# Kernel tuning notes

Hardware: AMD Instinct MI355X
Metric: run time of the kernel (lower is better)

The kernel has to match this reference:

```python
import jax, jax.numpy as jnp
import numpy as np

DIM = 64
SQRT_DIM = float(np.sqrt(DIM))


def setup_inputs() -> dict:
    rng = jax.random.key(0)
    k1, k2, k3, k4 = jax.random.split(rng, 4)
    B, S, D = 16, 2048, DIM
    query = jax.random.normal(k1, (B, S, D), dtype=jnp.float32)
    key = jax.random.normal(k2, (B, S, D), dtype=jnp.float32)
    value = jax.random.normal(k3, (B, S, D), dtype=jnp.float32)
    mask = jax.random.randint(k4, (B, S), 0, 2) == 1  # True = masked (pad)
    return {"query": query, "key": key, "value": value, "mask": mask}


def reference(query, key, value, mask):
    # score: [B, S, S]
    score = jnp.einsum('bsd,btd->bst', query, key) / SQRT_DIM
    # symmetric mask: position (i, j) masked if token i OR token j is padded
    m = jnp.logical_or(mask[:, :, None], mask[:, None, :])  # [B, S, S]
    score = jnp.where(m, -jnp.inf, score)
    attn = jax.nn.softmax(score, axis=-1)
    attn = jnp.where(m, 0.0, attn)
    context = jnp.einsum('bst,btd->bsd', attn, value)
    return (context, attn)
```

## Files before the change

kernel.cpp:

```cpp
#include <hip/hip_runtime.h>
#include <hip/hip_bf16.h>

#define NBATCH 16
#define SLEN   2048
#define DIM    64
#define TQ     64
#define NTHR   256
#define NW     4
#define PANEL  128
#define NPANEL (SLEN / PANEL)
#define PROWP  136
#define PROWK  72
#define PROWV  136

typedef __attribute__((ext_vector_type(8))) short bf16x8;
typedef __attribute__((ext_vector_type(4))) float f32x4;

__device__ inline short f2bf(float f) {
    union { __hip_bfloat16 h; short s; } u;
    u.h = __float2bfloat16(f);
    return u.s;
}
__device__ inline float bf2f(unsigned short s) {
    union { unsigned u; float f; } x;
    x.u = ((unsigned)s) << 16;
    return x.f;
}
__device__ inline bf16x8 pack8(float4 a, float4 b) {
    bf16x8 r;
    r[0] = f2bf(a.x); r[1] = f2bf(a.y); r[2] = f2bf(a.z); r[3] = f2bf(a.w);
    r[4] = f2bf(b.x); r[5] = f2bf(b.y); r[6] = f2bf(b.z); r[7] = f2bf(b.w);
    return r;
}
__device__ inline bf16x8 pack8s(float4 a, float4 b, float s) {
    bf16x8 r;
    r[0] = f2bf(a.x * s); r[1] = f2bf(a.y * s); r[2] = f2bf(a.z * s); r[3] = f2bf(a.w * s);
    r[4] = f2bf(b.x * s); r[5] = f2bf(b.y * s); r[6] = f2bf(b.z * s); r[7] = f2bf(b.w * s);
    return r;
}

__global__ __launch_bounds__(256) void preconvert_kernel(
    const float* __restrict__ K, const float* __restrict__ V,
    short* __restrict__ Kws, short* __restrict__ Vp)
{
    const int b  = blockIdx.x >> 4;
    const int p  = blockIdx.x & 15;
    const int j0 = p * PANEL;
    const int tid = threadIdx.x;
    const float* Kb = K + ((size_t)b * SLEN + j0) * DIM;
    const float* Vb = V + ((size_t)b * SLEN + j0) * DIM;
    short* Kwb = Kws + ((size_t)b * SLEN + j0) * DIM;
    short* Vpb = Vp  + (size_t)b * SLEN * DIM + (size_t)p * 8192;

    #pragma unroll
    for (int it = 0; it < 8; it++) {
        const int idx = it * 256 + tid;
        const int row = idx >> 4, c4 = idx & 15;
        float4 kv = *(const float4*)(Kb + (size_t)row * DIM + c4 * 4);
        const int blk = (c4 >> 1) ^ (row & 7);
        *(short4*)(Kwb + (size_t)row * DIM + blk * 8 + (c4 & 1) * 4) =
            make_short4(f2bf(kv.x), f2bf(kv.y), f2bf(kv.z), f2bf(kv.w));
    }
    #pragma unroll
    for (int it = 0; it < 2; it++) {
        const int task = it * 256 + tid;
        const int kb = (task >> 4) * 4, d4 = (task & 15) * 4;
        const float* vp = Vb + (size_t)kb * DIM + d4;
        float4 r0 = *(const float4*)(vp);
        float4 r1 = *(const float4*)(vp + DIM);
        float4 r2 = *(const float4*)(vp + 2 * DIM);
        float4 r3 = *(const float4*)(vp + 3 * DIM);
        const int ks = (kb >> 5) & 3, gg = (kb >> 3) & 3, e = kb & 7;
        #define VDST(dd) (Vpb + ((size_t)((ks * 4 + ((d4 + dd) >> 4)) * 64 \
                              + gg * 16 + ((d4 + dd) & 15))) * 8 + e)
        *(short4*)VDST(0) = make_short4(f2bf(r0.x), f2bf(r1.x), f2bf(r2.x), f2bf(r3.x));
        *(short4*)VDST(1) = make_short4(f2bf(r0.y), f2bf(r1.y), f2bf(r2.y), f2bf(r3.y));
        *(short4*)VDST(2) = make_short4(f2bf(r0.z), f2bf(r1.z), f2bf(r2.z), f2bf(r3.z));
        *(short4*)VDST(3) = make_short4(f2bf(r0.w), f2bf(r1.w), f2bf(r2.w), f2bf(r3.w));
        #undef VDST
    }
}

__device__ __forceinline__ void stage_k_panel(const short* __restrict__ Kwb, int j0,
                                              short* sdst, int w, int l) {
    const short* src = Kwb + (size_t)j0 * DIM + w * 512 + l * 8;
    short* dst = sdst + w * 512;
    #pragma unroll
    for (int i = 0; i < 4; i++)
        __builtin_amdgcn_global_load_lds((const unsigned int*)(src + i * 2048),
                                         (unsigned int*)(dst + i * 2048), 16, 0, 0);
}

#define MFMA16(a, bb, cc) __builtin_amdgcn_mfma_f32_16x16x32_bf16((a), (bb), (cc), 0, 0, 0)

__global__ __launch_bounds__(NTHR, 3) void sdpa_kernel(
    const float* __restrict__ Q, const short* __restrict__ Kws,
    const short* __restrict__ Vp, const int* __restrict__ M,
    float* __restrict__ outCtx, float* __restrict__ outAttn)
{
    __shared__ __align__(16) short sK0[PANEL * DIM];
    __shared__ __align__(16) short sK1[PANEL * DIM];
    __shared__ __align__(16) short sP[NW * 16 * PROWP];
    __shared__ short sMaskBf[SLEN];

    const int tid = threadIdx.x;
    const int w = tid >> 6, l = tid & 63, g = l >> 4, c = l & 15;
    const int wg = (blockIdx.x & 7) * (NBATCH * (SLEN / TQ) / 8) + (blockIdx.x >> 3);
    const int b  = wg >> 5;
    const int i0 = (wg & 31) * TQ;
    const int i0w = i0 + w * 16;

    const short* Kwb = Kws + (size_t)b * SLEN * DIM;
    const short* Vwb = Vp  + (size_t)b * SLEN * DIM;
    const int*   Mb  = M + b * SLEN;

    bf16x8 qa0, qa1;
    {
        const float* qp = Q + ((size_t)b * SLEN + i0w + c) * DIM + g * 8;
        qa0 = pack8s(*(const float4*)(qp),      *(const float4*)(qp + 4),  0.125f);
        qa1 = pack8s(*(const float4*)(qp + 32), *(const float4*)(qp + 36), 0.125f);
    }

    stage_k_panel(Kwb, 0, sK0, w, l);
    #pragma unroll
    for (int i = 0; i < 8; i++) {
        const int idx = i * NTHR + tid;
        sMaskBf[idx] = Mb[idx] ? (short)0 : (short)0x3F80;
    }
    __syncthreads();

    float rsum[4] = {0.f, 0.f, 0.f, 0.f};
    for (int p = 0; p < NPANEL; p++) {
        const short* cur = (p & 1) ? sK1 : sK0;
        if (p < NPANEL - 1)
            stage_k_panel(Kwb, (p + 1) * PANEL, (p & 1) ? sK0 : sK1, w, l);
        const int j0 = p * PANEL;
        #pragma unroll
        for (int jt = 0; jt < 8; jt++) {
            const short* kr = cur + (jt * 16 + c) * DIM;
            bf16x8 kb0 = *(const bf16x8*)(kr + ((g ^ (c & 7)) * 8));
            bf16x8 kb1 = *(const bf16x8*)(kr + (((g + 4) ^ (c & 7)) * 8));
            f32x4 acc = {0.f, 0.f, 0.f, 0.f};
            acc = MFMA16(qa0, kb0, acc);
            acc = MFMA16(qa1, kb1, acc);
            const float em = bf2f((unsigned short)sMaskBf[j0 + jt * 16 + c]);
            #pragma unroll
            for (int r = 0; r < 4; r++)
                rsum[r] += __expf(acc[r]) * em;
        }
        __syncthreads();
    }

    stage_k_panel(Kwb, 0, sK0, w, l);

    #pragma unroll
    for (int off = 1; off < 16; off <<= 1) {
        #pragma unroll
        for (int r = 0; r < 4; r++)
            rsum[r] += __shfl_xor(rsum[r], off, 64);
    }
    float scv[4];
    #pragma unroll
    for (int r = 0; r < 4; r++) {
        const bool rm = sMaskBf[i0w + g * 4 + r] == 0;
        scv[r] = (rm || rsum[r] <= 0.f) ? 0.f : 1.f / rsum[r];
    }

    short* sPw = sP + w * 16 * PROWP;
    f32x4 pv[4];
    #pragma unroll
    for (int nt = 0; nt < 4; nt++) pv[nt] = (f32x4){0.f, 0.f, 0.f, 0.f};

    __syncthreads();

    for (int p = 0; p < NPANEL; p++) {
        const int j0 = p * PANEL;
        if (p < NPANEL - 1)
            stage_k_panel(Kwb, j0 + PANEL, (p & 1) ? sK0 : sK1, w, l);
        const short* kbuf = (p & 1) ? sK1 : sK0;

        #pragma unroll
        for (int jt = 0; jt < 8; jt++) {
            const short* kr = kbuf + (jt * 16 + c) * DIM;
            bf16x8 kb0 = *(const bf16x8*)(kr + ((g ^ (c & 7)) * 8));
            bf16x8 kb1 = *(const bf16x8*)(kr + (((g + 4) ^ (c & 7)) * 8));
            f32x4 acc = {0.f, 0.f, 0.f, 0.f};
            acc = MFMA16(qa0, kb0, acc);
            acc = MFMA16(qa1, kb1, acc);
            const float em = bf2f((unsigned short)sMaskBf[j0 + jt * 16 + c]);
            #pragma unroll
            for (int r = 0; r < 4; r++)
                sPw[(g * 4 + r) * PROWP + jt * 16 + c] =
                    f2bf(__expf(acc[r]) * em * scv[r]);
        }
        {
            const short* vb = Vwb + (size_t)p * 8192 + l * 8;
            bf16x8 v0 = *(const bf16x8*)(vb);
            bf16x8 v1 = *(const bf16x8*)(vb + 512);
            bf16x8 af;
            #pragma unroll
            for (int i = 0; i < 16; i++) {
                bf16x8 cur = v0;
                v0 = v1;
                if (i + 2 < 16) v1 = *(const bf16x8*)(vb + (i + 2) * 512);
                if ((i & 3) == 0)
                    af = *(const bf16x8*)(sPw + c * PROWP + (i >> 2) * 32 + g * 8);
                pv[i & 3] = MFMA16(af, cur, pv[i & 3]);
            }
        }
        const size_t rowBase = (size_t)b * SLEN + i0w;
        #pragma unroll
        for (int it = 0; it < 8; it++) {
            const int idx = it * 64 + l;
            const int row = idx >> 5, col4 = idx & 31;
            const unsigned short* pp = (const unsigned short*)sPw + row * PROWP + col4 * 4;
            ushort4 p4 = *(const ushort4*)(pp);
            f32x4 o = {bf2f(p4.x), bf2f(p4.y), bf2f(p4.z), bf2f(p4.w)};
            __builtin_nontemporal_store(o,
                (f32x4*)(outAttn + (rowBase + row) * SLEN + j0 + col4 * 4));
        }
        __syncthreads();
    }

    #pragma unroll
    for (int nt = 0; nt < 4; nt++) {
        #pragma unroll
        for (int r = 0; r < 4; r++)
            __builtin_nontemporal_store(pv[nt][r],
                outCtx + ((size_t)b * SLEN + i0w + g * 4 + r) * DIM + nt * 16 + c);
    }
}

__global__ __launch_bounds__(NTHR, 3) void sdpa_kernel_fb(
    const float* __restrict__ Q, const float* __restrict__ K,
    const float* __restrict__ V, const int* __restrict__ M,
    float* __restrict__ outCtx, float* __restrict__ outAttn)
{
    __shared__ __align__(16) short sK[128 * PROWK];
    __shared__ __align__(16) short sVT[64 * PROWV];
    __shared__ __align__(16) short sP[NW * 16 * PROWP];
    __shared__ float sMask[PANEL];

    const int tid = threadIdx.x;
    const int w = tid >> 6, l = tid & 63, g = l >> 4, c = l & 15;
    const int b  = blockIdx.x >> 5;
    const int i0 = (blockIdx.x & 31) * TQ;
    const int i0w = i0 + w * 16;

    const float* Kb = K + (size_t)b * SLEN * DIM;
    const float* Vb = V + (size_t)b * SLEN * DIM;
    const int*   Mb = M + b * SLEN;

    bf16x8 qa0, qa1;
    {
        const float* qp = Q + ((size_t)b * SLEN + i0w + c) * DIM + g * 8;
        qa0 = pack8(*(const float4*)(qp),      *(const float4*)(qp + 4));
        qa1 = pack8(*(const float4*)(qp + 32), *(const float4*)(qp + 36));
    }

    const float scl = 0.125f;
    float rsum[4] = {0.f, 0.f, 0.f, 0.f};

    for (int p = 0; p < NPANEL; p++) {
        const int j0 = p * PANEL;
        #pragma unroll
        for (int it = 0; it < 8; it++) {
            const int idx = it * NTHR + tid;
            const int row = idx >> 4, c4 = idx & 15;
            float4 kv = *(const float4*)(Kb + (size_t)(j0 + row) * DIM + c4 * 4);
            *(short4*)(sK + row * PROWK + c4 * 4) =
                make_short4(f2bf(kv.x), f2bf(kv.y), f2bf(kv.z), f2bf(kv.w));
        }
        if (tid < PANEL) sMask[tid] = Mb[j0 + tid] ? 0.f : 1.f;
        __syncthreads();
        #pragma unroll
        for (int jt = 0; jt < 8; jt++) {
            const short* kr = sK + (jt * 16 + c) * PROWK + g * 8;
            bf16x8 kb0 = *(const bf16x8*)(kr);
            bf16x8 kb1 = *(const bf16x8*)(kr + 32);
            f32x4 acc = {0.f, 0.f, 0.f, 0.f};
            acc = MFMA16(qa0, kb0, acc);
            acc = MFMA16(qa1, kb1, acc);
            const float em = sMask[jt * 16 + c];
            #pragma unroll
            for (int r = 0; r < 4; r++)
                rsum[r] += __expf(acc[r] * scl) * em;
        }
        __syncthreads();
    }
    #pragma unroll
    for (int off = 1; off < 16; off <<= 1) {
        #pragma unroll
        for (int r = 0; r < 4; r++)
            rsum[r] += __shfl_xor(rsum[r], off, 64);
    }
    float scv[4];
    #pragma unroll
    for (int r = 0; r < 4; r++) {
        const int rm = Mb[i0w + g * 4 + r];
        scv[r] = (rm || rsum[r] <= 0.f) ? 0.f : 1.f / rsum[r];
    }

    short* sPw = sP + w * 16 * PROWP;
    f32x4 pv[4];
    #pragma unroll
    for (int nt = 0; nt < 4; nt++) pv[nt] = (f32x4){0.f, 0.f, 0.f, 0.f};

    for (int p = 0; p < NPANEL; p++) {
        const int j0 = p * PANEL;
        #pragma unroll
        for (int it = 0; it < 8; it++) {
            const int idx = it * NTHR + tid;
            const int row = idx >> 4, c4 = idx & 15;
            float4 kv = *(const float4*)(Kb + (size_t)(j0 + row) * DIM + c4 * 4);
            *(short4*)(sK + row * PROWK + c4 * 4) =
                make_short4(f2bf(kv.x), f2bf(kv.y), f2bf(kv.z), f2bf(kv.w));
        }
        #pragma unroll
        for (int it = 0; it < 2; it++) {
            const int task = it * NTHR + tid;
            const int k4 = task >> 4, d4g = task & 15;
            const int kb = k4 * 4, d4 = d4g * 4;
            const int colb = kb ^ ((d4g & 3) << 3);
            const float* vp = Vb + (size_t)(j0 + kb) * DIM + d4;
            float4 r0 = *(const float4*)(vp);
            float4 r1 = *(const float4*)(vp + DIM);
            float4 r2 = *(const float4*)(vp + 2 * DIM);
            float4 r3 = *(const float4*)(vp + 3 * DIM);
            *(short4*)(sVT + (d4 + 0) * PROWV + colb) =
                make_short4(f2bf(r0.x), f2bf(r1.x), f2bf(r2.x), f2bf(r3.x));
            *(short4*)(sVT + (d4 + 1) * PROWV + colb) =
                make_short4(f2bf(r0.y), f2bf(r1.y), f2bf(r2.y), f2bf(r3.y));
            *(short4*)(sVT + (d4 + 2) * PROWV + colb) =
                make_short4(f2bf(r0.z), f2bf(r1.z), f2bf(r2.z), f2bf(r3.z));
            *(short4*)(sVT + (d4 + 3) * PROWV + colb) =
                make_short4(f2bf(r0.w), f2bf(r1.w), f2bf(r2.w), f2bf(r3.w));
        }
        if (tid < PANEL) sMask[tid] = Mb[j0 + tid] ? 0.f : 1.f;
        __syncthreads();

        #pragma unroll
        for (int jt = 0; jt < 8; jt++) {
            const short* kr = sK + (jt * 16 + c) * PROWK + g * 8;
            bf16x8 kb0 = *(const bf16x8*)(kr);
            bf16x8 kb1 = *(const bf16x8*)(kr + 32);
            f32x4 acc = {0.f, 0.f, 0.f, 0.f};
            acc = MFMA16(qa0, kb0, acc);
            acc = MFMA16(qa1, kb1, acc);
            const float em = sMask[jt * 16 + c];
            #pragma unroll
            for (int r = 0; r < 4; r++)
                sPw[(g * 4 + r) * PROWP + jt * 16 + c] =
                    f2bf(__expf(acc[r] * scl) * em * scv[r]);
        }
        #pragma unroll
        for (int ks = 0; ks < 4; ks++) {
            bf16x8 af = *(const bf16x8*)(sPw + c * PROWP + ks * 32 + g * 8);
            #pragma unroll
            for (int nt = 0; nt < 4; nt++) {
                const int d = nt * 16 + c;
                const int gp = g ^ ((d >> 2) & 3);
                bf16x8 bfrag = *(const bf16x8*)(sVT + d * PROWV + ks * 32 + gp * 8);
                pv[nt] = MFMA16(af, bfrag, pv[nt]);
            }
        }
        const size_t rowBase = (size_t)b * SLEN + i0w;
        #pragma unroll
        for (int it = 0; it < 8; it++) {
            const int idx = it * 64 + l;
            const int row = idx >> 5, col4 = idx & 31;
            const unsigned short* pp = (const unsigned short*)sPw + row * PROWP + col4 * 4;
            ushort4 p4 = *(const ushort4*)(pp);
            float4 o = {bf2f(p4.x), bf2f(p4.y), bf2f(p4.z), bf2f(p4.w)};
            *(float4*)(outAttn + (rowBase + row) * SLEN + j0 + col4 * 4) = o;
        }
        __syncthreads();
    }

    #pragma unroll
    for (int nt = 0; nt < 4; nt++) {
        #pragma unroll
        for (int r = 0; r < 4; r++)
            outCtx[((size_t)b * SLEN + i0w + g * 4 + r) * DIM + nt * 16 + c] = pv[nt][r];
    }
}

extern "C" void kernel_launch(void* const* d_in, const int* in_sizes, int n_in,
                              void* d_out, int out_size, void* d_ws, size_t ws_size,
                              hipStream_t stream) {
    const float* Q = (const float*)d_in[0];
    const float* K = (const float*)d_in[1];
    const float* V = (const float*)d_in[2];
    const int*   M = (const int*)d_in[3];
    float* outCtx  = (float*)d_out;
    float* outAttn = (float*)d_out + (size_t)NBATCH * SLEN * DIM;
    dim3 grid(NBATCH * (SLEN / TQ));

    const size_t nElem = (size_t)NBATCH * SLEN * DIM;
    const size_t wsNeed = nElem * 2 * sizeof(short);
    if (d_ws != nullptr && ws_size >= wsNeed) {
        short* Kws = (short*)d_ws;
        short* Vpp = Kws + nElem;
        preconvert_kernel<<<dim3(NBATCH * NPANEL), 256, 0, stream>>>(K, V, Kws, Vpp);
        sdpa_kernel<<<grid, NTHR, 0, stream>>>(Q, Kws, Vpp, M, outCtx, outAttn);
    } else {
        sdpa_kernel_fb<<<grid, NTHR, 0, stream>>>(Q, K, V, M, outCtx, outAttn);
    }
}
```

Before: 311.2 us.

## Transpose QK MFMA so each lane owns a query row and stores attn directly

The QK^T MFMA operands are swapped so the accumulator holds four consecutive key columns for one query row per lane. The row sum then needs only two cross-lane shuffles, and the mask reads become vectorized short4 loads. Attention probabilities are written to global memory straight from fp32 registers with 16-byte nontemporal stores. This removes the old readback of bf16 values from shared memory and the bf16 round-trip in the attn output. PV MFMAs are interleaved with QK tiles, with V loads prefetched per k-step, at the cost of more live registers.

```diff
diff --git a/kernel.cpp b/kernel.cpp
--- a/kernel.cpp
+++ b/kernel.cpp
@@ -129,7 +129,7 @@
     }
     __syncthreads();
 
-    float rsum[4] = {0.f, 0.f, 0.f, 0.f};
+    float rsum = 0.f;
     for (int p = 0; p < NPANEL; p++) {
         const short* cur = (p & 1) ? sK1 : sK0;
         if (p < NPANEL - 1)
@@ -141,30 +141,23 @@
             bf16x8 kb0 = *(const bf16x8*)(kr + ((g ^ (c & 7)) * 8));
             bf16x8 kb1 = *(const bf16x8*)(kr + (((g + 4) ^ (c & 7)) * 8));
             f32x4 acc = {0.f, 0.f, 0.f, 0.f};
-            acc = MFMA16(qa0, kb0, acc);
-            acc = MFMA16(qa1, kb1, acc);
-            const float em = bf2f((unsigned short)sMaskBf[j0 + jt * 16 + c]);
-            #pragma unroll
-            for (int r = 0; r < 4; r++)
-                rsum[r] += __expf(acc[r]) * em;
+            acc = MFMA16(kb0, qa0, acc);
+            acc = MFMA16(kb1, qa1, acc);
+            short4 m4 = *(const short4*)(sMaskBf + j0 + jt * 16 + g * 4);
+            rsum += __expf(acc[0]) * bf2f((unsigned short)m4.x)
+                  + __expf(acc[1]) * bf2f((unsigned short)m4.y)
+                  + __expf(acc[2]) * bf2f((unsigned short)m4.z)
+                  + __expf(acc[3]) * bf2f((unsigned short)m4.w);
         }
         __syncthreads();
     }
 
     stage_k_panel(Kwb, 0, sK0, w, l);
 
-    #pragma unroll
-    for (int off = 1; off < 16; off <<= 1) {
-        #pragma unroll
-        for (int r = 0; r < 4; r++)
-            rsum[r] += __shfl_xor(rsum[r], off, 64);
-    }
-    float scv[4];
-    #pragma unroll
-    for (int r = 0; r < 4; r++) {
-        const bool rm = sMaskBf[i0w + g * 4 + r] == 0;
-        scv[r] = (rm || rsum[r] <= 0.f) ? 0.f : 1.f / rsum[r];
-    }
+    rsum += __shfl_xor(rsum, 16, 64);
+    rsum += __shfl_xor(rsum, 32, 64);
+    const bool rm = sMaskBf[i0w + c] == 0;
+    const float scv = (rm || rsum <= 0.f) ? 0.f : 1.f / rsum;
 
     short* sPw = sP + w * 16 * PROWP;
     f32x4 pv[4];
@@ -178,46 +171,51 @@
         if (p < NPANEL - 1)
             stage_k_panel(Kwb, j0 + PANEL, (p & 1) ? sK0 : sK1, w, l);
         const short* kbuf = (p & 1) ? sK1 : sK0;
-
-        #pragma unroll
-        for (int jt = 0; jt < 8; jt++) {
-            const short* kr = kbuf + (jt * 16 + c) * DIM;
-            bf16x8 kb0 = *(const bf16x8*)(kr + ((g ^ (c & 7)) * 8));
-            bf16x8 kb1 = *(const bf16x8*)(kr + (((g + 4) ^ (c & 7)) * 8));
-            f32x4 acc = {0.f, 0.f, 0.f, 0.f};
-            acc = MFMA16(qa0, kb0, acc);
-            acc = MFMA16(qa1, kb1, acc);
-            const float em = bf2f((unsigned short)sMaskBf[j0 + jt * 16 + c]);
+        const short* vb = Vwb + (size_t)p * 8192 + l * 8;
+
+        bf16x8 vc0 = *(const bf16x8*)(vb);
+        bf16x8 vc1 = *(const bf16x8*)(vb + 512);
+        bf16x8 vc2 = *(const bf16x8*)(vb + 1024);
+        bf16x8 vc3 = *(const bf16x8*)(vb + 1536);
+
+        const size_t rowB = ((size_t)b * SLEN + i0w + c) * SLEN + j0;
+
+        #pragma unroll
+        for (int ks = 0; ks < 4; ks++) {
+            bf16x8 vn0, vn1, vn2, vn3;
+            if (ks < 3) {
+                const short* vnb = vb + (ks + 1) * 2048;
+                vn0 = *(const bf16x8*)(vnb);
+                vn1 = *(const bf16x8*)(vnb + 512);
+                vn2 = *(const bf16x8*)(vnb + 1024);
+                vn3 = *(const bf16x8*)(vnb + 1536);
+            }
             #pragma unroll
-            for (int r = 0; r < 4; r++)
-                sPw[(g * 4 + r) * PROWP + jt * 16 + c] =
-                    f2bf(__expf(acc[r]) * em * scv[r]);
-        }
-        {
-            const short* vb = Vwb + (size_t)p * 8192 + l * 8;
-            bf16x8 v0 = *(const bf16x8*)(vb);
-            bf16x8 v1 = *(const bf16x8*)(vb + 512);
-            bf16x8 af;
-            #pragma unroll
-            for (int i = 0; i < 16; i++) {
-                bf16x8 cur = v0;
-                v0 = v1;
-                if (i + 2 < 16) v1 = *(const bf16x8*)(vb + (i + 2) * 512);
-                if ((i & 3) == 0)
-                    af = *(const bf16x8*)(sPw + c * PROWP + (i >> 2) * 32 + g * 8);
-                pv[i & 3] = MFMA16(af, cur, pv[i & 3]);
+            for (int jj = 0; jj < 2; jj++) {
+                const int jt = ks * 2 + jj;
+                const short* kr = kbuf + (jt * 16 + c) * DIM;
+                bf16x8 kb0 = *(const bf16x8*)(kr + ((g ^ (c & 7)) * 8));
+                bf16x8 kb1 = *(const bf16x8*)(kr + (((g + 4) ^ (c & 7)) * 8));
+                f32x4 acc = {0.f, 0.f, 0.f, 0.f};
+                acc = MFMA16(kb0, qa0, acc);
+                acc = MFMA16(kb1, qa1, acc);
+                short4 m4 = *(const short4*)(sMaskBf + j0 + jt * 16 + g * 4);
+                f32x4 pr;
+                pr[0] = __expf(acc[0]) * bf2f((unsigned short)m4.x) * scv;
+                pr[1] = __expf(acc[1]) * bf2f((unsigned short)m4.y) * scv;
+                pr[2] = __expf(acc[2]) * bf2f((unsigned short)m4.z) * scv;
+                pr[3] = __expf(acc[3]) * bf2f((unsigned short)m4.w) * scv;
+                __builtin_nontemporal_store(pr,
+                    (f32x4*)(outAttn + rowB + jt * 16 + g * 4));
+                *(short4*)(sPw + c * PROWP + jt * 16 + g * 4) =
+                    make_short4(f2bf(pr[0]), f2bf(pr[1]), f2bf(pr[2]), f2bf(pr[3]));
             }
-        }
-        const size_t rowBase = (size_t)b * SLEN + i0w;
-        #pragma unroll
-        for (int it = 0; it < 8; it++) {
-            const int idx = it * 64 + l;
-            const int row = idx >> 5, col4 = idx & 31;
-            const unsigned short* pp = (const unsigned short*)sPw + row * PROWP + col4 * 4;
-            ushort4 p4 = *(const ushort4*)(pp);
-            f32x4 o = {bf2f(p4.x), bf2f(p4.y), bf2f(p4.z), bf2f(p4.w)};
-            __builtin_nontemporal_store(o,
-                (f32x4*)(outAttn + (rowBase + row) * SLEN + j0 + col4 * 4));
+            bf16x8 af = *(const bf16x8*)(sPw + c * PROWP + ks * 32 + g * 8);
+            pv[0] = MFMA16(af, vc0, pv[0]);
+            pv[1] = MFMA16(af, vc1, pv[1]);
+            pv[2] = MFMA16(af, vc2, pv[2]);
+            pv[3] = MFMA16(af, vc3, pv[3]);
+            if (ks < 3) { vc0 = vn0; vc1 = vn1; vc2 = vn2; vc3 = vn3; }
         }
         __syncthreads();
     }
```

Measured after the change: 347.4 us. +11.6%, slower.
